# Performance work log

Hardware: AMD Instinct MI355X
Metric: run time of the kernel (lower is better)

## Reference

```python
import jax, jax.numpy as jnp
import numpy as np

B, N, C, L = 32, 1024, 128, 4

def setup_inputs() -> dict:
    key = jax.random.key(0)
    ks = jax.random.split(key, 8)
    x = jax.random.normal(ks[0], (B, N, C), dtype=jnp.float32)
    # binary adjacency: nonzero entries become unit-weight edges (edge weights unused in module)
    adj = jax.random.randint(ks[1], (B, N, N), 0, 2).astype(jnp.float32)
    mask = jnp.ones((B, N), dtype=jnp.float32)
    s = 1.0 / np.sqrt(C)
    weight = jax.random.uniform(ks[2], (L, C, C), minval=-s, maxval=s, dtype=jnp.float32)
    w_ih = jax.random.uniform(ks[3], (L, 3 * C, C), minval=-s, maxval=s, dtype=jnp.float32)
    w_hh = jax.random.uniform(ks[4], (L, 3 * C, C), minval=-s, maxval=s, dtype=jnp.float32)
    b_ih = jax.random.uniform(ks[5], (L, 3 * C), minval=-s, maxval=s, dtype=jnp.float32)
    b_hh = jax.random.uniform(ks[6], (L, 3 * C), minval=-s, maxval=s, dtype=jnp.float32)
    return {"x": x, "adj": adj, "mask": mask, "weight": weight,
            "w_ih": w_ih, "w_hh": w_hh, "b_ih": b_ih, "b_hh": b_hh}

def _gru_cell(m, h, w_ih, w_hh, b_ih, b_hh):
    # PyTorch GRUCell, gate order (r, z, n)
    gx = m @ w_ih.T + b_ih
    gh = h @ w_hh.T + b_hh
    xr, xz, xn = jnp.split(gx, 3, axis=-1)
    hr, hz, hn = jnp.split(gh, 3, axis=-1)
    r = jax.nn.sigmoid(xr + hr)
    z = jax.nn.sigmoid(xz + hz)
    n = jnp.tanh(xn + r * hn)
    return (1.0 - z) * n + z * h

def reference(x, adj, mask, weight, w_ih, w_hh, b_ih, b_hh):
    h = x  # [B, N, C]; in_channels == out_channels so no zero-padding needed
    for i in range(L):
        hw = jnp.einsum('bnc,cd->bnd', h, weight[i])
        # scatter-add of messages source->target == A^T @ (h W), unit edge weights
        m = jnp.einsum('bjn,bjd->bnd', adj, hw)
        h = _gru_cell(m, h, w_ih[i], w_hh[i], b_ih[i], b_hh[i])
    return h * mask[:, :, None]
```

## Files before the change

### kernel.cpp

```cpp
#include <hip/hip_runtime.h>
#include <stdint.h>


#define NB 32
#define NN 1024
#define NC 128
#define NL 4
#define MTOT (NB * NN)

#define KT 64
#define PITCH 72

typedef __attribute__((ext_vector_type(8))) short s16x8;
typedef __attribute__((ext_vector_type(4))) float f32x4;
typedef __attribute__((ext_vector_type(2))) unsigned int u32x2;
typedef unsigned short U16;
typedef unsigned int U32;

__device__ __forceinline__ U16 f2bf(float f) {
    union { float f; U32 u; } v; v.f = f;
    return (U16)((v.u + 0x7FFFu + ((v.u >> 16) & 1u)) >> 16);
}
__device__ __forceinline__ float bf2f(U16 h) {
    union { U32 u; float f; } v; v.u = ((U32)h) << 16;
    return v.f;
}
__device__ __forceinline__ void splitbf(float x, U16& hi, U16& lo) {
    hi = f2bf(x);
    lo = f2bf(x - bf2f(hi));
}
__device__ __forceinline__ float sigmoidf_(float x) { return 1.f / (1.f + __expf(-x)); }

__device__ __forceinline__ void glds16(const void* g, void* l) {
    __builtin_amdgcn_global_load_lds(
        (const __attribute__((address_space(1))) void*)g,
        (__attribute__((address_space(3))) void*)l, 16, 0, 0);
}

#define SWZ(row, g) ((row) * 64 + ((((g) ^ ((row) & 7))) * 8))

__global__ __launch_bounds__(256) void k_setup(
    const float* __restrict__ adj, U16* __restrict__ adjT,
    const float* __restrict__ w, const float* __restrict__ wih, const float* __restrict__ whh,
    U16* __restrict__ wThi, U16* __restrict__ wTlo,
    U16* __restrict__ wihhi, U16* __restrict__ wihlo,
    U16* __restrict__ whhhi, U16* __restrict__ whhlo,
    const float* __restrict__ x, U16* __restrict__ hhi, U16* __restrict__ hlo)
{
    __shared__ float t[64 * 65];
    const int bid = blockIdx.x, tid = threadIdx.x;
    if (bid < 8192) {
        const int b = bid >> 8, rem = bid & 255;
        const int j0 = (rem & 15) * 64, n0 = (rem >> 4) * 64;
        const int rr = tid >> 4, c4 = (tid & 15) * 4;
#pragma unroll
        for (int p = 0; p < 4; ++p) {
            int j = p * 16 + rr;
            f32x4 v = *(const f32x4*)&adj[((size_t)b << 20) + ((size_t)(j0 + j) << 10) + n0 + c4];
#pragma unroll
            for (int u = 0; u < 4; ++u) t[j * 65 + c4 + u] = v[u];
        }
        __syncthreads();
#pragma unroll
        for (int p = 0; p < 4; ++p) {
            int n = p * 16 + rr;
            U16 h0 = f2bf(t[(c4 + 0) * 65 + n]);
            U16 h1 = f2bf(t[(c4 + 1) * 65 + n]);
            U16 h2 = f2bf(t[(c4 + 2) * 65 + n]);
            U16 h3 = f2bf(t[(c4 + 3) * 65 + n]);
            u32x2 pk; pk[0] = (U32)h0 | ((U32)h1 << 16); pk[1] = (U32)h2 | ((U32)h3 << 16);
            *(u32x2*)&adjT[((size_t)b << 20) + ((size_t)(n0 + n) << 10) + j0 + c4] = pk;
        }
    } else if (bid < 9984) {
        int i = (bid - 8192) * 256 + tid;
        if (i < 65536) {
            int l = i >> 14, rem = i & 16383, c = rem >> 7, d = rem & 127;
            U16 hi, lo; splitbf(w[i], hi, lo);
            int o = (l << 14) + (d << 7) + c;
            wThi[o] = hi; wTlo[o] = lo;
        } else if (i < 262144) {
            int j = i - 65536;
            U16 hi, lo; splitbf(wih[j], hi, lo);
            wihhi[j] = hi; wihlo[j] = lo;
        } else {
            int j = i - 262144;
            U16 hi, lo; splitbf(whh[j], hi, lo);
            whhhi[j] = hi; whhlo[j] = lo;
        }
    } else {
        int base = (bid - 9984) * 2048 + tid;
#pragma unroll
        for (int p = 0; p < 8; ++p) {
            int i = base + p * 256;
            U16 hi, lo; splitbf(x[i], hi, lo);
            hhi[i] = hi; hlo[i] = lo;
        }
    }
}

struct __align__(16) Smem3 {
    union {
        struct { U16 A[2][128 * PITCH]; U16 B[2][128 * PITCH]; } s;
        float bounce[128 * 129];
    };
};

__global__ __launch_bounds__(256, 2) void k_hw(
    const U16* __restrict__ Ahi, const U16* __restrict__ Alo,
    const U16* __restrict__ Bhi, const U16* __restrict__ Blo,
    U16* __restrict__ Ohi, U16* __restrict__ Olo)
{
    __shared__ Smem3 sm;
    const int tid = threadIdx.x;
    const int lane = tid & 63, wv = tid >> 6;
    const int wr = (wv & 1) * 64, wc = (wv >> 1) * 64;
    const int lm = lane & 15, lk8 = (lane >> 4) * 8;
    const int m0 = blockIdx.x * 128;

    f32x4 acc[4][4] = {};

    for (int kc = 0; kc < 128; kc += KT) {
#pragma unroll
        for (int t = 0; t < 4; ++t) {
            int i = tid + t * 256; int r = i >> 3, v = (i & 7) * 8;
            *(s16x8*)&sm.s.A[0][r * PITCH + v] = *(const s16x8*)&Ahi[(size_t)(m0 + r) * 128 + kc + v];
            *(s16x8*)&sm.s.A[1][r * PITCH + v] = *(const s16x8*)&Alo[(size_t)(m0 + r) * 128 + kc + v];
        }
#pragma unroll
        for (int t = 0; t < 4; ++t) {
            int i = tid + t * 256; int r = i >> 3, v = (i & 7) * 8;
            *(s16x8*)&sm.s.B[0][r * PITCH + v] = *(const s16x8*)&Bhi[r * 128 + kc + v];
            *(s16x8*)&sm.s.B[1][r * PITCH + v] = *(const s16x8*)&Blo[r * 128 + kc + v];
        }
        __syncthreads();
#pragma unroll
        for (int ks = 0; ks < 2; ++ks) {
            const int ko = ks * 32 + lk8;
            s16x8 ahi[4], alo[4], bhi[4], blo[4];
#pragma unroll
            for (int q = 0; q < 4; ++q) {
                ahi[q] = *(const s16x8*)&sm.s.A[0][(wr + q * 16 + lm) * PITCH + ko];
                alo[q] = *(const s16x8*)&sm.s.A[1][(wr + q * 16 + lm) * PITCH + ko];
                bhi[q] = *(const s16x8*)&sm.s.B[0][(wc + q * 16 + lm) * PITCH + ko];
                blo[q] = *(const s16x8*)&sm.s.B[1][(wc + q * 16 + lm) * PITCH + ko];
            }
#pragma unroll
            for (int rt = 0; rt < 4; ++rt)
#pragma unroll
                for (int ct = 0; ct < 4; ++ct) {
                    f32x4 a = acc[rt][ct];
                    a = __builtin_amdgcn_mfma_f32_16x16x32_bf16(ahi[rt], bhi[ct], a, 0, 0, 0);
                    a = __builtin_amdgcn_mfma_f32_16x16x32_bf16(ahi[rt], blo[ct], a, 0, 0, 0);
                    a = __builtin_amdgcn_mfma_f32_16x16x32_bf16(alo[rt], bhi[ct], a, 0, 0, 0);
                    acc[rt][ct] = a;
                }
        }
        __syncthreads();
    }
#pragma unroll
    for (int rt = 0; rt < 4; ++rt)
#pragma unroll
        for (int ct = 0; ct < 4; ++ct)
#pragma unroll
            for (int r = 0; r < 4; ++r)
                sm.bounce[(wr + rt * 16 + (lane >> 4) * 4 + r) * 129 + wc + ct * 16 + lm] = acc[rt][ct][r];
    __syncthreads();
    const int b = m0 >> 10, j0 = m0 & 1023;
    for (int t = 0; t < 32; ++t) {
        int i = tid + t * 256; int d = i >> 6, j2 = (i & 63) * 2;
        float x0 = sm.bounce[j2 * 129 + d], x1 = sm.bounce[(j2 + 1) * 129 + d];
        U16 h0, l0, h1, l1; splitbf(x0, h0, l0); splitbf(x1, h1, l1);
        size_t o = (((size_t)(b * 128 + d)) << 10) + j0 + j2;
        *(U32*)&Ohi[o] = (U32)h0 | ((U32)h1 << 16);
        *(U32*)&Olo[o] = (U32)l0 | ((U32)l1 << 16);
    }
}

__global__ __launch_bounds__(256, 2) void k_mega4(
    const U16* __restrict__ adjT,
    const U16* __restrict__ hwThi, const U16* __restrict__ hwTlo,
    U16* mhi, U16* mlo,
    const U16* __restrict__ hhi, const U16* __restrict__ hlo,
    const U16* __restrict__ wihhi, const U16* __restrict__ wihlo,
    const U16* __restrict__ whhhi, const U16* __restrict__ whhlo,
    const float* __restrict__ bih, const float* __restrict__ bhh,
    const float* __restrict__ mask,
    U16* __restrict__ houthi, U16* __restrict__ houtlo,
    float* __restrict__ out, int last)
{
    __shared__ U16 As[2][64 * 64];
    __shared__ U16 Bh[2][128 * 64];
    __shared__ U16 Bl[2][128 * 64];
    const int tid = threadIdx.x;
    const int lane = tid & 63, wv = tid >> 6;
    const int wd0 = wv * 32;
    const int lm = lane & 15, lk8 = (lane >> 4) * 8, quad = lane >> 4;
    const int xcd = blockIdx.x & 7;
    const int j = blockIdx.x >> 3;
    const int bt = xcd * 4 + (j >> 4);
    const int n0 = (j & 15) * 64;
    const int row0 = bt * NN + n0;

#define STAGE(kc, b)                                                                     \
    {                                                                                    \
        _Pragma("unroll")                                                                \
        for (int t = 0; t < 2; ++t) {                                                    \
            int li = tid + t * 256; int r = li >> 3, sg = li & 7;                        \
            glds16(&adjT[((size_t)bt << 20) + ((size_t)(n0 + r) << 10) + (kc)            \
                         + ((sg ^ (r & 7)) * 8)],                                        \
                   &As[b][li * 8]);                                                      \
        }                                                                                \
        _Pragma("unroll")                                                                \
        for (int t = 0; t < 4; ++t) {                                                    \
            int li = tid + t * 256; int d = li >> 3, sg = li & 7;                        \
            size_t o = (((size_t)(bt * 128 + d)) << 10) + (kc) + ((sg ^ (d & 7)) * 8);   \
            glds16(&hwThi[o], &Bh[b][li * 8]);                                           \
            glds16(&hwTlo[o], &Bl[b][li * 8]);                                           \
        }                                                                                \
    }

    f32x4 macc[4][2] = {};
    STAGE(0, 0);
    for (int c = 0; c < 16; ++c) {
        const int b = c & 1;
        __syncthreads();
        if (c + 1 < 16) STAGE((c + 1) * 64, b ^ 1);
#pragma unroll
        for (int ks = 0; ks < 2; ++ks) {
            const int g = ks * 4 + quad;
            s16x8 a[4], bh[2], bl[2];
#pragma unroll
            for (int q = 0; q < 4; ++q)
                a[q] = *(const s16x8*)&As[b][SWZ(q * 16 + lm, g)];
#pragma unroll
            for (int q = 0; q < 2; ++q) {
                bh[q] = *(const s16x8*)&Bh[b][SWZ(wd0 + q * 16 + lm, g)];
                bl[q] = *(const s16x8*)&Bl[b][SWZ(wd0 + q * 16 + lm, g)];
            }
#pragma unroll
            for (int rt = 0; rt < 4; ++rt)
#pragma unroll
                for (int ct = 0; ct < 2; ++ct) {
                    f32x4 cc = macc[rt][ct];
                    cc = __builtin_amdgcn_mfma_f32_16x16x32_bf16(a[rt], bh[ct], cc, 0, 0, 0);
                    cc = __builtin_amdgcn_mfma_f32_16x16x32_bf16(a[rt], bl[ct], cc, 0, 0, 0);
                    macc[rt][ct] = cc;
                }
        }
    }
#undef STAGE

#pragma unroll
    for (int rt = 0; rt < 4; ++rt)
#pragma unroll
        for (int ct = 0; ct < 2; ++ct)
#pragma unroll
            for (int rr = 0; rr < 4; ++rr) {
                int rloc = rt * 16 + quad * 4 + rr;
                int d = wd0 + ct * 16 + lm;
                U16 hi, lo; splitbf(macc[rt][ct][rr], hi, lo);
                size_t o = (size_t)(row0 + rloc) * 128 + d;
                mhi[o] = hi; mlo[o] = lo;
            }

    f32x4 aR[4][2], aZ[4][2], aXN[4][2], aHN[4][2];
#pragma unroll
    for (int ct = 0; ct < 2; ++ct) {
        const int col = wd0 + ct * 16 + lm;
        const float bR  = bih[col]       + bhh[col];
        const float bZ  = bih[128 + col] + bhh[128 + col];
        const float bXN = bih[256 + col];
        const float bHN = bhh[256 + col];
#pragma unroll
        for (int rt = 0; rt < 4; ++rt) {
            aR[rt][ct]  = f32x4{bR, bR, bR, bR};
            aZ[rt][ct]  = f32x4{bZ, bZ, bZ, bZ};
            aXN[rt][ct] = f32x4{bXN, bXN, bXN, bXN};
            aHN[rt][ct] = f32x4{bHN, bHN, bHN, bHN};
        }
    }

    for (int cc = 0; cc < 4; ++cc) {
        const int ch = (cc + 2) & 3;
        if (cc == 2) __syncthreads();
        const U16* Ahi = (ch < 2) ? (const U16*)mhi : hhi;
        const U16* Alo = (ch < 2) ? (const U16*)mlo : hlo;
        const U16* __restrict__ Whi = (ch < 2) ? wihhi : whhhi;
        const U16* __restrict__ Wlo = (ch < 2) ? wihlo : whhlo;
        const int kb = (ch & 1) * 64;
#pragma unroll
        for (int ks = 0; ks < 2; ++ks) {
            const int ko = kb + ks * 32 + lk8;
            s16x8 ahi[4], alo[4];
#pragma unroll
            for (int q = 0; q < 4; ++q) {
                size_t ao = (size_t)(row0 + q * 16 + lm) * 128 + ko;
                ahi[q] = *(const s16x8*)&Ahi[ao];
                alo[q] = *(const s16x8*)&Alo[ao];
            }
#pragma unroll
            for (int ct = 0; ct < 2; ++ct) {
                const int col = wd0 + ct * 16 + lm;
                s16x8 bhiR = *(const s16x8*)&Whi[(size_t)col * 128 + ko];
                s16x8 bloR = *(const s16x8*)&Wlo[(size_t)col * 128 + ko];
                s16x8 bhiZ = *(const s16x8*)&Whi[(size_t)(128 + col) * 128 + ko];
                s16x8 bloZ = *(const s16x8*)&Wlo[(size_t)(128 + col) * 128 + ko];
                s16x8 bhiN = *(const s16x8*)&Whi[(size_t)(256 + col) * 128 + ko];
                s16x8 bloN = *(const s16x8*)&Wlo[(size_t)(256 + col) * 128 + ko];
#pragma unroll
                for (int rt = 0; rt < 4; ++rt) {
                    f32x4 r = aR[rt][ct];
                    r = __builtin_amdgcn_mfma_f32_16x16x32_bf16(ahi[rt], bhiR, r, 0, 0, 0);
                    r = __builtin_amdgcn_mfma_f32_16x16x32_bf16(ahi[rt], bloR, r, 0, 0, 0);
                    r = __builtin_amdgcn_mfma_f32_16x16x32_bf16(alo[rt], bhiR, r, 0, 0, 0);
                    aR[rt][ct] = r;
                    f32x4 z = aZ[rt][ct];
                    z = __builtin_amdgcn_mfma_f32_16x16x32_bf16(ahi[rt], bhiZ, z, 0, 0, 0);
                    z = __builtin_amdgcn_mfma_f32_16x16x32_bf16(ahi[rt], bloZ, z, 0, 0, 0);
                    z = __builtin_amdgcn_mfma_f32_16x16x32_bf16(alo[rt], bhiZ, z, 0, 0, 0);
                    aZ[rt][ct] = z;
                }
                if (ch < 2) {
#pragma unroll
                    for (int rt = 0; rt < 4; ++rt) {
                        f32x4 n = aXN[rt][ct];
                        n = __builtin_amdgcn_mfma_f32_16x16x32_bf16(ahi[rt], bhiN, n, 0, 0, 0);
                        n = __builtin_amdgcn_mfma_f32_16x16x32_bf16(ahi[rt], bloN, n, 0, 0, 0);
                        n = __builtin_amdgcn_mfma_f32_16x16x32_bf16(alo[rt], bhiN, n, 0, 0, 0);
                        aXN[rt][ct] = n;
                    }
                } else {
#pragma unroll
                    for (int rt = 0; rt < 4; ++rt) {
                        f32x4 n = aHN[rt][ct];
                        n = __builtin_amdgcn_mfma_f32_16x16x32_bf16(ahi[rt], bhiN, n, 0, 0, 0);
                        n = __builtin_amdgcn_mfma_f32_16x16x32_bf16(ahi[rt], bloN, n, 0, 0, 0);
                        n = __builtin_amdgcn_mfma_f32_16x16x32_bf16(alo[rt], bhiN, n, 0, 0, 0);
                        aHN[rt][ct] = n;
                    }
                }
            }
        }
    }

#pragma unroll
    for (int rt = 0; rt < 4; ++rt) {
#pragma unroll
        for (int ct = 0; ct < 2; ++ct) {
            const int col = wd0 + ct * 16 + lm;
#pragma unroll
            for (int rr = 0; rr < 4; ++rr) {
                const int row = row0 + rt * 16 + quad * 4 + rr;
                float r = sigmoidf_(aR[rt][ct][rr]);
                float z = sigmoidf_(aZ[rt][ct][rr]);
                float n = tanhf(aXN[rt][ct][rr] + r * aHN[rt][ct][rr]);
                size_t ho = (size_t)row * 128 + col;
                float hv = bf2f(hhi[ho]) + bf2f(hlo[ho]);
                float hnew = (1.f - z) * n + z * hv;
                if (last) {
                    out[ho] = hnew * mask[row];
                } else {
                    U16 hi2, lo2; splitbf(hnew, hi2, lo2);
                    houthi[ho] = hi2;
                    houtlo[ho] = lo2;
                }
            }
        }
    }
}

extern "C" void kernel_launch(void* const* d_in, const int* in_sizes, int n_in,
                              void* d_out, int out_size, void* d_ws, size_t ws_size,
                              hipStream_t stream) {
    (void)in_sizes; (void)n_in; (void)out_size; (void)ws_size;
    const float* x    = (const float*)d_in[0];
    const float* adj  = (const float*)d_in[1];
    const float* mask = (const float*)d_in[2];
    const float* wgt  = (const float*)d_in[3];
    const float* wih  = (const float*)d_in[4];
    const float* whh  = (const float*)d_in[5];
    const float* bih  = (const float*)d_in[6];
    const float* bhh  = (const float*)d_in[7];
    float* out = (float*)d_out;

    char* p = (char*)d_ws;
    U16* adjT    = (U16*)p;                p += (size_t)NB * NN * NN * 2;
    U16* h_hi    = (U16*)p;                p += (size_t)MTOT * NC * 2;
    U16* h_lo    = (U16*)p;                p += (size_t)MTOT * NC * 2;
    U16* hwT_hi  = (U16*)p;                p += (size_t)NB * NC * NN * 2;
    U16* hwT_lo  = (U16*)p;                p += (size_t)NB * NC * NN * 2;
    U16* m_hi    = (U16*)p;                p += (size_t)MTOT * NC * 2;
    U16* m_lo    = (U16*)p;                p += (size_t)MTOT * NC * 2;
    U16* wT_hi   = (U16*)p;                p += (size_t)NL * NC * NC * 2;
    U16* wT_lo   = (U16*)p;                p += (size_t)NL * NC * NC * 2;
    U16* wih_hi  = (U16*)p;                p += (size_t)NL * 384 * NC * 2;
    U16* wih_lo  = (U16*)p;                p += (size_t)NL * 384 * NC * 2;
    U16* whh_hi  = (U16*)p;                p += (size_t)NL * 384 * NC * 2;
    U16* whh_lo  = (U16*)p;                p += (size_t)NL * 384 * NC * 2;

    k_setup<<<12032, 256, 0, stream>>>(adj, adjT, wgt, wih, whh,
                                       wT_hi, wT_lo, wih_hi, wih_lo, whh_hi, whh_lo,
                                       x, h_hi, h_lo);

    for (int l = 0; l < NL; ++l) {
        k_hw<<<256, 256, 0, stream>>>(h_hi, h_lo,
                                      wT_hi + l * 16384, wT_lo + l * 16384,
                                      hwT_hi, hwT_lo);
        k_mega4<<<512, 256, 0, stream>>>(adjT, hwT_hi, hwT_lo, m_hi, m_lo, h_hi, h_lo,
                                         wih_hi + l * 49152, wih_lo + l * 49152,
                                         whh_hi + l * 49152, whh_lo + l * 49152,
                                         bih + l * 384, bhh + l * 384, mask,
                                         h_hi, h_lo, out, (l == NL - 1) ? 1 : 0);
    }
}
```

Baseline: 600.5 us.

## Halve row tile to 32 and drop LDS double buffering for higher occupancy

The fused aggregation+GRU kernel now processes 32 node rows per block instead of 64, launching 1024 blocks instead of 512. Shared memory drops to a single buffer, and the register footprint halves, so launch bounds rise to four blocks per CU. The cost is that the global-to-LDS staging no longer overlaps with MFMA compute, which adds a barrier per chunk. The hw and weight tiles are also re-read twice as often per output row.

```diff
diff --git a/kernel.cpp b/kernel.cpp
--- a/kernel.cpp
+++ b/kernel.cpp
@@ -176,7 +176,7 @@
     }
 }
 
-__global__ __launch_bounds__(256, 2) void k_mega4(
+__global__ __launch_bounds__(256, 4) void k_mega5(
     const U16* __restrict__ adjT,
     const U16* __restrict__ hwThi, const U16* __restrict__ hwTlo,
     U16* mhi, U16* mlo,
@@ -188,57 +188,54 @@
     U16* __restrict__ houthi, U16* __restrict__ houtlo,
     float* __restrict__ out, int last)
 {
-    __shared__ U16 As[2][64 * 64];
-    __shared__ U16 Bh[2][128 * 64];
-    __shared__ U16 Bl[2][128 * 64];
+    __shared__ U16 As[32 * 64];
+    __shared__ U16 Bh[128 * 64];
+    __shared__ U16 Bl[128 * 64];
     const int tid = threadIdx.x;
     const int lane = tid & 63, wv = tid >> 6;
     const int wd0 = wv * 32;
     const int lm = lane & 15, lk8 = (lane >> 4) * 8, quad = lane >> 4;
     const int xcd = blockIdx.x & 7;
     const int j = blockIdx.x >> 3;
-    const int bt = xcd * 4 + (j >> 4);
-    const int n0 = (j & 15) * 64;
+    const int bt = xcd * 4 + (j >> 5);
+    const int n0 = (j & 31) * 32;
     const int row0 = bt * NN + n0;
 
-#define STAGE(kc, b)                                                                     \
+#define STAGE(kc)                                                                        \
     {                                                                                    \
-        _Pragma("unroll")                                                                \
-        for (int t = 0; t < 2; ++t) {                                                    \
-            int li = tid + t * 256; int r = li >> 3, sg = li & 7;                        \
+        {                                                                                \
+            int r = tid >> 3, sg = tid & 7;                                              \
             glds16(&adjT[((size_t)bt << 20) + ((size_t)(n0 + r) << 10) + (kc)            \
                          + ((sg ^ (r & 7)) * 8)],                                        \
-                   &As[b][li * 8]);                                                      \
+                   &As[tid * 8]);                                                        \
         }                                                                                \
         _Pragma("unroll")                                                                \
         for (int t = 0; t < 4; ++t) {                                                    \
             int li = tid + t * 256; int d = li >> 3, sg = li & 7;                        \
             size_t o = (((size_t)(bt * 128 + d)) << 10) + (kc) + ((sg ^ (d & 7)) * 8);   \
-            glds16(&hwThi[o], &Bh[b][li * 8]);                                           \
-            glds16(&hwTlo[o], &Bl[b][li * 8]);                                           \
+            glds16(&hwThi[o], &Bh[li * 8]);                                              \
+            glds16(&hwTlo[o], &Bl[li * 8]);                                              \
         }                                                                                \
     }
 
-    f32x4 macc[4][2] = {};
-    STAGE(0, 0);
+    f32x4 macc[2][2] = {};
     for (int c = 0; c < 16; ++c) {
-        const int b = c & 1;
+        STAGE(c * 64);
         __syncthreads();
-        if (c + 1 < 16) STAGE((c + 1) * 64, b ^ 1);
 #pragma unroll
         for (int ks = 0; ks < 2; ++ks) {
             const int g = ks * 4 + quad;
-            s16x8 a[4], bh[2], bl[2];
-#pragma unroll
-            for (int q = 0; q < 4; ++q)
-                a[q] = *(const s16x8*)&As[b][SWZ(q * 16 + lm, g)];
+            s16x8 a[2], bh[2], bl[2];
+#pragma unroll
+            for (int q = 0; q < 2; ++q)
+                a[q] = *(const s16x8*)&As[SWZ(q * 16 + lm, g)];
 #pragma unroll
             for (int q = 0; q < 2; ++q) {
-                bh[q] = *(const s16x8*)&Bh[b][SWZ(wd0 + q * 16 + lm, g)];
-                bl[q] = *(const s16x8*)&Bl[b][SWZ(wd0 + q * 16 + lm, g)];
-            }
-#pragma unroll
-            for (int rt = 0; rt < 4; ++rt)
+                bh[q] = *(const s16x8*)&Bh[SWZ(wd0 + q * 16 + lm, g)];
+                bl[q] = *(const s16x8*)&Bl[SWZ(wd0 + q * 16 + lm, g)];
+            }
+#pragma unroll
+            for (int rt = 0; rt < 2; ++rt)
 #pragma unroll
                 for (int ct = 0; ct < 2; ++ct) {
                     f32x4 cc = macc[rt][ct];
@@ -247,11 +244,12 @@
                     macc[rt][ct] = cc;
                 }
         }
+        __syncthreads();
     }
 #undef STAGE
 
 #pragma unroll
-    for (int rt = 0; rt < 4; ++rt)
+    for (int rt = 0; rt < 2; ++rt)
 #pragma unroll
         for (int ct = 0; ct < 2; ++ct)
 #pragma unroll
@@ -263,7 +261,7 @@
                 mhi[o] = hi; mlo[o] = lo;
             }
 
-    f32x4 aR[4][2], aZ[4][2], aXN[4][2], aHN[4][2];
+    f32x4 aR[2][2], aZ[2][2], aXN[2][2], aHN[2][2];
 #pragma unroll
     for (int ct = 0; ct < 2; ++ct) {
         const int col = wd0 + ct * 16 + lm;
@@ -272,7 +270,7 @@
         const float bXN = bih[256 + col];
         const float bHN = bhh[256 + col];
 #pragma unroll
-        for (int rt = 0; rt < 4; ++rt) {
+        for (int rt = 0; rt < 2; ++rt) {
             aR[rt][ct]  = f32x4{bR, bR, bR, bR};
             aZ[rt][ct]  = f32x4{bZ, bZ, bZ, bZ};
             aXN[rt][ct] = f32x4{bXN, bXN, bXN, bXN};
@@ -291,9 +289,9 @@
 #pragma unroll
         for (int ks = 0; ks < 2; ++ks) {
             const int ko = kb + ks * 32 + lk8;
-            s16x8 ahi[4], alo[4];
-#pragma unroll
-            for (int q = 0; q < 4; ++q) {
+            s16x8 ahi[2], alo[2];
+#pragma unroll
+            for (int q = 0; q < 2; ++q) {
                 size_t ao = (size_t)(row0 + q * 16 + lm) * 128 + ko;
                 ahi[q] = *(const s16x8*)&Ahi[ao];
                 alo[q] = *(const s16x8*)&Alo[ao];
@@ -308,7 +306,7 @@
                 s16x8 bhiN = *(const s16x8*)&Whi[(size_t)(256 + col) * 128 + ko];
                 s16x8 bloN = *(const s16x8*)&Wlo[(size_t)(256 + col) * 128 + ko];
 #pragma unroll
-                for (int rt = 0; rt < 4; ++rt) {
+                for (int rt = 0; rt < 2; ++rt) {
                     f32x4 r = aR[rt][ct];
                     r = __builtin_amdgcn_mfma_f32_16x16x32_bf16(ahi[rt], bhiR, r, 0, 0, 0);
                     r = __builtin_amdgcn_mfma_f32_16x16x32_bf16(ahi[rt], bloR, r, 0, 0, 0);
@@ -322,7 +320,7 @@
                 }
                 if (ch < 2) {
 #pragma unroll
-                    for (int rt = 0; rt < 4; ++rt) {
+                    for (int rt = 0; rt < 2; ++rt) {
                         f32x4 n = aXN[rt][ct];
                         n = __builtin_amdgcn_mfma_f32_16x16x32_bf16(ahi[rt], bhiN, n, 0, 0, 0);
                         n = __builtin_amdgcn_mfma_f32_16x16x32_bf16(ahi[rt], bloN, n, 0, 0, 0);
@@ -331,7 +329,7 @@
                     }
                 } else {
 #pragma unroll
-                    for (int rt = 0; rt < 4; ++rt) {
+                    for (int rt = 0; rt < 2; ++rt) {
                         f32x4 n = aHN[rt][ct];
                         n = __builtin_amdgcn_mfma_f32_16x16x32_bf16(ahi[rt], bhiN, n, 0, 0, 0);
                         n = __builtin_amdgcn_mfma_f32_16x16x32_bf16(ahi[rt], bloN, n, 0, 0, 0);
@@ -344,7 +342,7 @@
     }
 
 #pragma unroll
-    for (int rt = 0; rt < 4; ++rt) {
+    for (int rt = 0; rt < 2; ++rt) {
 #pragma unroll
         for (int ct = 0; ct < 2; ++ct) {
             const int col = wd0 + ct * 16 + lm;
@@ -406,10 +404,10 @@
         k_hw<<<256, 256, 0, stream>>>(h_hi, h_lo,
                                       wT_hi + l * 16384, wT_lo + l * 16384,
                                       hwT_hi, hwT_lo);
-        k_mega4<<<512, 256, 0, stream>>>(adjT, hwT_hi, hwT_lo, m_hi, m_lo, h_hi, h_lo,
-                                         wih_hi + l * 49152, wih_lo + l * 49152,
-                                         whh_hi + l * 49152, whh_lo + l * 49152,
-                                         bih + l * 384, bhh + l * 384, mask,
-                                         h_hi, h_lo, out, (l == NL - 1) ? 1 : 0);
-    }
-}
+        k_mega5<<<1024, 256, 0, stream>>>(adjT, hwT_hi, hwT_lo, m_hi, m_lo, h_hi, h_lo,
+                                          wih_hi + l * 49152, wih_lo + l * 49152,
+                                          whh_hi + l * 49152, whh_lo + l * 49152,
+                                          bih + l * 384, bhh + l * 384, mask,
+                                          h_hi, h_lo, out, (l == NL - 1) ? 1 : 0);
+    }
+}
```

Measured after the change: 654.6 us. +9.0%, slower.
